# Kernel optimization log

Hardware: AMD Instinct MI355X
Metric: run time of the kernel (lower is better)

The kernel has to match this reference:

```python
import jax, jax.numpy as jnp
import numpy as np

C_DIM = 128
HIDDEN = 128
RESO = 128
PADDING = 0.1


def _resnet_block(x, w0, b0, w1, b1, ws):
    # ResnetBlockFC: net = fc_0(relu(x)); dx = fc_1(relu(net)); out = shortcut(x) + dx
    net = jnp.maximum(x, 0.0) @ w0 + b0
    dx = jnp.maximum(net, 0.0) @ w1 + b1
    return x @ ws + dx


def _scatter_mean(c, index, num_seg):
    # c: (B, T, C) float, index: (B, T) int -> (B, num_seg, C), empty bins stay 0
    def one(cb, ib):
        s = jax.ops.segment_sum(cb, ib, num_segments=num_seg)
        cnt = jax.ops.segment_sum(jnp.ones((cb.shape[0],), cb.dtype), ib, num_segments=num_seg)
        return s / jnp.maximum(cnt, 1.0)[:, None]
    return jax.vmap(one)(c, index)


def setup_inputs() -> dict:
    key = jax.random.key(0)
    ks = jax.random.split(key, 12)
    B, T, D = 2, 65536, 3
    h = HIDDEN
    p = jax.random.uniform(ks[0], (B, T, D), jnp.float32, minval=-0.5, maxval=0.5)
    s = 0.02
    fc_pos_w = jax.random.normal(ks[1], (D, 2 * h), jnp.float32) * s
    fc_pos_b = jax.random.normal(ks[2], (2 * h,), jnp.float32) * s
    # 5 ResnetBlockFC blocks, all (2h -> h) since c_dim == hidden_dim
    w0 = jax.random.normal(ks[3], (5, 2 * h, h), jnp.float32) * s
    b0 = jax.random.normal(ks[4], (5, h), jnp.float32) * s
    w1 = jax.random.normal(ks[5], (5, h, h), jnp.float32) * s
    b1 = jax.random.normal(ks[6], (5, h), jnp.float32) * s
    ws = jax.random.normal(ks[7], (5, 2 * h, h), jnp.float32) * s  # shortcut, no bias
    return {"p": p, "fc_pos_w": fc_pos_w, "fc_pos_b": fc_pos_b,
            "w0": w0, "b0": b0, "w1": w1, "b1": b1, "ws": ws}


def reference(p, fc_pos_w, fc_pos_b, w0, b0, w1, b1, ws):
    # PointNet ResNet encoder
    net = p @ fc_pos_w + fc_pos_b  # (B, T, 2h)
    for i in range(5):
        hfeat = _resnet_block(net, w0[i], b0[i], w1[i], b1[i], ws[i])  # (B, T, h)
        if i < 4:
            pooled = jnp.max(hfeat, axis=1, keepdims=True)
            net = jnp.concatenate([hfeat, jnp.broadcast_to(pooled, hfeat.shape)], axis=-1)
    c = hfeat  # (B, T, c_dim)

    # normalize_coordinate(plane='xz'): take dims (0, 2), map to [0, 1)
    xy = p[..., jnp.array([0, 2])]
    xy = xy / (1.0 + PADDING + 1e-3) + 0.5
    xy = jnp.clip(xy, 0.0, 1.0 - 1e-6)
    # coordinate2index
    xi = (xy * RESO).astype(jnp.int32)
    index = xi[..., 0] + RESO * xi[..., 1]  # (B, T)

    fea = _scatter_mean(c, index, RESO * RESO)  # (B, R*R, c_dim)
    fea_plane = jnp.transpose(fea, (0, 2, 1)).reshape(p.shape[0], C_DIM, RESO, RESO)
    return fea_plane
```

## Files before the change

kernel.cpp:

```cpp
#include <hip/hip_runtime.h>
#include <hip/hip_bf16.h>


#define G_ALL 131072
#define HD    128
#define NBINS 16384

typedef __attribute__((ext_vector_type(8))) short short8;
typedef __attribute__((ext_vector_type(4))) float f32x4;

#define MFMA16(a, b, c) __builtin_amdgcn_mfma_f32_16x16x32_bf16(a, b, c, 0, 0, 0)

__device__ __forceinline__ float bf16_to_f32(unsigned short u) {
  union { unsigned int u; float f; } v; v.u = ((unsigned int)u) << 16; return v.f;
}
__device__ __forceinline__ unsigned short f32_to_bf16(float f) {
  union { float f; unsigned int u; } v; v.f = f;
  unsigned int u = v.u;
  u += 0x7fffu + ((u >> 16) & 1u);
  return (unsigned short)(u >> 16);
}
__device__ __forceinline__ unsigned int f32_key(float f) {
  union { float f; unsigned int u; } v; v.f = f;
  return (v.u & 0x80000000u) ? ~v.u : (v.u | 0x80000000u);
}
__device__ __forceinline__ float key_f32(unsigned int k) {
  union { unsigned int u; float f; } v;
  v.u = (k & 0x80000000u) ? (k & 0x7fffffffu) : ~k;
  return v.f;
}
__device__ __forceinline__ int bin_of(float p0, float p2) {
  float x = p0 / 1.101f + 0.5f;
  x = fminf(fmaxf(x, 0.0f), 1.0f - 1e-6f);
  int xi = (int)(x * 128.0f);
  float z = p2 / 1.101f + 0.5f;
  z = fminf(fmaxf(z, 0.0f), 1.0f - 1e-6f);
  int zi = (int)(z * 128.0f);
  return xi + 128 * zi;
}
__device__ __forceinline__ short8 relu8(short8 a) {
  short8 r;
#pragma unroll
  for (int e = 0; e < 8; e++) r[e] = a[e] < 0 ? (short)0 : a[e];
  return r;
}

__global__ void prep_kernel(const float* __restrict__ fcw,
                            const float* __restrict__ fcb,
                            const float* __restrict__ ws0,
                            float* __restrict__ Sp, float* __restrict__ bsp,
                            unsigned int* __restrict__ pool,
                            int* __restrict__ hist) {
  int j = threadIdx.x;
  for (int d = 0; d < 3; d++) {
    float s = 0.f;
    for (int ch = 0; ch < 256; ch++)
      s = fmaf(fcw[d * 256 + ch], ws0[ch * HD + j], s);
    Sp[d * HD + j] = s;
  }
  float s = 0.f;
  for (int ch = 0; ch < 256; ch++)
    s = fmaf(fcb[ch], ws0[ch * HD + j], s);
  bsp[j] = s;
  for (int k = j; k < 4 * 2 * 128; k += 128) pool[k] = 0u;
  for (int k = j; k < 2 * NBINS; k += 128) hist[k] = 0;
}

__global__ void wprep_kernel(const float* __restrict__ w0,
                             const float* __restrict__ w1,
                             const float* __restrict__ ws,
                             unsigned short* __restrict__ B0t,
                             unsigned short* __restrict__ W0t,
                             unsigned short* __restrict__ W1t,
                             unsigned short* __restrict__ WSt) {
  int gid = blockIdx.x * 256 + threadIdx.x;
  float v;
  unsigned short* dstp;
  int dst;
  if (gid < 32768) {
    int n = gid >> 8, k = gid & 255;
    v = w0[k * 128 + n];
    dstp = B0t; dst = gid;
  } else if (gid < 98304) {
    int i = gid - 32768; int s = i >> 14; int n = (i >> 7) & 127; int k = i & 127;
    v = w0[(size_t)((s + 1) * 256 + k) * 128 + n];
    dstp = W0t; dst = i;
  } else if (gid < 180224) {
    int i = gid - 98304; int s = i >> 14; int n = (i >> 7) & 127; int k = i & 127;
    v = w1[(size_t)(s * 128 + k) * 128 + n];
    dstp = W1t; dst = i;
  } else if (gid < 245760) {
    int i = gid - 180224; int s = i >> 14; int n = (i >> 7) & 127; int k = i & 127;
    v = ws[(size_t)((s + 1) * 256 + k) * 128 + n];
    dstp = WSt; dst = i;
  } else return;
  dstp[dst] = f32_to_bf16(v);
}

__global__ __launch_bounds__(256) void index_kernel(const float* __restrict__ p,
                                                    int* __restrict__ hist) {
  int g = blockIdx.x * 256 + threadIdx.x;
  int b = g >> 16;
  int idx = bin_of(p[3 * (size_t)g], p[3 * (size_t)g + 2]);
  atomicAdd(&hist[b * NBINS + idx], 1);
}

__global__ __launch_bounds__(1024) void scan_kernel(int* __restrict__ hist,
                                                    int* __restrict__ offsets) {
  __shared__ int sd[1024];
  int t = threadIdx.x;
  int vals[32];
  int s = 0;
#pragma unroll
  for (int i = 0; i < 32; i++) { vals[i] = hist[t * 32 + i]; s += vals[i]; }
  sd[t] = s;
  __syncthreads();
  for (int d = 1; d < 1024; d <<= 1) {
    int v = (t >= d) ? sd[t - d] : 0;
    __syncthreads();
    sd[t] += v;
    __syncthreads();
  }
  int run = sd[t] - s;
#pragma unroll
  for (int i = 0; i < 32; i++) {
    offsets[t * 32 + i] = run;
    hist[t * 32 + i] = run;
    run += vals[i];
  }
  if (t == 1023) offsets[32768] = run;
}

__global__ __launch_bounds__(256) void fill_kernel(const float* __restrict__ p,
                                                   int* __restrict__ cursor,
                                                   int* __restrict__ order) {
  int g = blockIdx.x * 256 + threadIdx.x;
  int b = g >> 16;
  int idx = bin_of(p[3 * (size_t)g], p[3 * (size_t)g + 2]);
  int pos = atomicAdd(&cursor[b * NBINS + idx], 1);
  order[pos] = g;
}

__global__ __launch_bounds__(256) void gather_kernel(
    const unsigned short* __restrict__ c, const int* __restrict__ offsets,
    const int* __restrict__ order, float* __restrict__ out) {
  __shared__ float acc[129 * 65];
  const int tid = threadIdx.x;
  const int wave = tid >> 6, lane = tid & 63;
  const int B0 = blockIdx.x * 64;
  const int b = B0 >> 14;

  for (int bi = 0; bi < 16; bi++) {
    const int binL = wave * 16 + bi;
    const int B = B0 + binL;
    const int st = offsets[B], en = offsets[B + 1];
    float a0 = 0.f, a1 = 0.f;
    for (int k = st; k < en; k++) {
      int g = order[k];
      unsigned int u = *(const unsigned int*)(c + (size_t)g * HD + lane * 2);
      a0 += bf16_to_f32((unsigned short)(u & 0xffffu));
      a1 += bf16_to_f32((unsigned short)(u >> 16));
    }
    acc[(2 * lane) * 65 + binL] = a0;
    acc[(2 * lane + 1) * 65 + binL] = a1;
    if (lane == 0) acc[128 * 65 + binL] = (float)(en - st);
  }
  __syncthreads();

  const size_t outBase = (size_t)b * HD * NBINS + (size_t)(B0 & (NBINS - 1));
  const float cnt = fmaxf(acc[128 * 65 + lane], 1.0f);
#pragma unroll
  for (int c2 = 0; c2 < 32; c2++) {
    int ch = wave * 32 + c2;
    out[outBase + (size_t)ch * NBINS + lane] = acc[ch * 65 + lane] / cnt;
  }
}

__global__ __launch_bounds__(512, 4) void stage0_kernel(
    const float* __restrict__ p, const float* __restrict__ fcw,
    const float* __restrict__ fcb,
    const unsigned short* __restrict__ B0t,
    const unsigned short* __restrict__ W1t,
    const float* __restrict__ b0, const float* __restrict__ b1,
    const float* __restrict__ Sp, const float* __restrict__ bsp,
    unsigned short* __restrict__ hout, unsigned int* __restrict__ pool) {
  __shared__ float fcL[1024];
  __shared__ float ptL[64 * 5];
  __shared__ unsigned short x0t[64 * 264];
  __shared__ unsigned short m2[64 * 136];
  const int tid = threadIdx.x;
  const int lane = tid & 63;
  const int q = lane >> 4, l15 = lane & 15;
  const int nt = tid >> 6;
  const int b = blockIdx.x >> 8;
  const int wrow = nt * 16 + l15;

  short8 b0w[8], w1w[4];
#pragma unroll
  for (int kc = 0; kc < 8; kc++)
    b0w[kc] = *(const short8*)(B0t + (size_t)wrow * 256 + kc * 32 + q * 8);
#pragma unroll
  for (int kc = 0; kc < 4; kc++)
    w1w[kc] = *(const short8*)(W1t + (size_t)wrow * 128 + kc * 32 + q * 8);
  const float bias1 = b0[wrow];
  const float bias2 = bsp[wrow] + b1[wrow];
  const float sp0 = Sp[wrow], sp1 = Sp[128 + wrow], sp2 = Sp[256 + wrow];

  for (int k = tid; k < 1024; k += 512)
    fcL[k] = (k < 768) ? fcw[k] : fcb[k - 768];

  for (int it = 0; it < 4; it++) {
    const int rowBase = (blockIdx.x * 4 + it) * 64;
    __syncthreads();
    if (tid < 192) ptL[(tid / 3) * 5 + (tid % 3)] = p[(size_t)rowBase * 3 + tid];
    {
      int row = tid >> 3, c8 = tid & 7;
      const float* pr = p + (size_t)(rowBase + row) * 3;
      float p0 = pr[0], p1 = pr[1], p2 = pr[2];
#pragma unroll
      for (int cc = 0; cc < 32; cc++) {
        int ch = c8 + cc * 8;
        float x = fcL[768 + ch] + p0 * fcL[ch] + p1 * fcL[256 + ch] + p2 * fcL[512 + ch];
        x0t[row * 264 + ch] = f32_to_bf16(fmaxf(x, 0.f));
      }
    }
    __syncthreads();
    f32x4 C1[4];
#pragma unroll
    for (int s = 0; s < 4; s++) C1[s] = (f32x4){bias1, bias1, bias1, bias1};
#pragma unroll
    for (int kc = 0; kc < 8; kc++) {
#pragma unroll
      for (int s = 0; s < 4; s++) {
        short8 Ar = *(const short8*)(&x0t[(s * 16 + l15) * 264 + kc * 32 + q * 8]);
        C1[s] = MFMA16(Ar, b0w[kc], C1[s]);
      }
    }
#pragma unroll
    for (int s = 0; s < 4; s++)
#pragma unroll
      for (int r = 0; r < 4; r++)
        m2[(s * 16 + q * 4 + r) * 136 + nt * 16 + l15] =
            f32_to_bf16(fmaxf(C1[s][r], 0.f));
    __syncthreads();
    f32x4 C2[4];
#pragma unroll
    for (int s = 0; s < 4; s++)
#pragma unroll
      for (int r = 0; r < 4; r++) {
        int row = s * 16 + q * 4 + r;
        C2[s][r] = bias2 + ptL[row * 5] * sp0 + ptL[row * 5 + 1] * sp1 +
                   ptL[row * 5 + 2] * sp2;
      }
#pragma unroll
    for (int kc = 0; kc < 4; kc++) {
#pragma unroll
      for (int s = 0; s < 4; s++) {
        short8 Am = *(const short8*)(&m2[(s * 16 + l15) * 136 + kc * 32 + q * 8]);
        C2[s] = MFMA16(Am, w1w[kc], C2[s]);
      }
    }
#pragma unroll
    for (int s = 0; s < 4; s++)
#pragma unroll
      for (int r = 0; r < 4; r++)
        x0t[(s * 16 + q * 4 + r) * 136 + nt * 16 + l15] = f32_to_bf16(C2[s][r]);
    {
      float m = -1e30f;
#pragma unroll
      for (int s = 0; s < 4; s++)
#pragma unroll
        for (int r = 0; r < 4; r++) m = fmaxf(m, C2[s][r]);
      m = fmaxf(m, __shfl_xor(m, 16, 64));
      m = fmaxf(m, __shfl_xor(m, 32, 64));
      if (lane < 16) atomicMax(&pool[b * 128 + nt * 16 + lane], f32_key(m));
    }
    __syncthreads();
    {
      int r = tid >> 3, cs = (tid & 7) * 16;
      short8 v0 = *(const short8*)(&x0t[r * 136 + cs]);
      short8 v1 = *(const short8*)(&x0t[r * 136 + cs + 8]);
      *(short8*)(hout + (size_t)(rowBase + r) * 128 + cs) = v0;
      *(short8*)(hout + (size_t)(rowBase + r) * 128 + cs + 8) = v1;
    }
  }
}

__global__ __launch_bounds__(512, 4) void stageN_kernel(
    const unsigned short* __restrict__ hin, unsigned short* __restrict__ hout,
    const unsigned short* __restrict__ W0t,
    const unsigned short* __restrict__ W1t,
    const unsigned short* __restrict__ WSt,
    const float* __restrict__ b0e, const float* __restrict__ bse,
    unsigned int* __restrict__ pool, int doPool) {
  __shared__ unsigned short At[64 * 136];
  __shared__ unsigned short m2[64 * 136];
  const int tid = threadIdx.x;
  const int lane = tid & 63;
  const int q = lane >> 4, l15 = lane & 15;
  const int nt = tid >> 6;
  const int b = blockIdx.x >> 8;
  const int wrow = nt * 16 + l15;

  short8 w0w[4], w1w[4], wsw[4];
#pragma unroll
  for (int kc = 0; kc < 4; kc++) {
    w0w[kc] = *(const short8*)(W0t + (size_t)wrow * 128 + kc * 32 + q * 8);
    w1w[kc] = *(const short8*)(W1t + (size_t)wrow * 128 + kc * 32 + q * 8);
    wsw[kc] = *(const short8*)(WSt + (size_t)wrow * 128 + kc * 32 + q * 8);
  }
  const float bias1 = b0e[b * 128 + wrow];
  const float bias2 = bse[b * 128 + wrow];
  const int r8 = tid >> 3, cs8 = (tid & 7) * 16;

  for (int it = 0; it < 4; it++) {
    const int rowBase = (blockIdx.x * 4 + it) * 64;
    __syncthreads();
    {
      const size_t gb = ((size_t)rowBase + r8) * 128 + cs8;
      short8 v0 = *(const short8*)(hin + gb);
      short8 v1 = *(const short8*)(hin + gb + 8);
      *(short8*)(&At[r8 * 136 + cs8]) = v0;
      *(short8*)(&At[r8 * 136 + cs8 + 8]) = v1;
    }
    __syncthreads();
    f32x4 C1[4], C2[4];
#pragma unroll
    for (int s = 0; s < 4; s++) {
      C1[s] = (f32x4){bias1, bias1, bias1, bias1};
      C2[s] = (f32x4){bias2, bias2, bias2, bias2};
    }
#pragma unroll
    for (int kc = 0; kc < 4; kc++) {
#pragma unroll
      for (int s = 0; s < 4; s++) {
        short8 Ah = *(const short8*)(&At[(s * 16 + l15) * 136 + kc * 32 + q * 8]);
        short8 Ar = relu8(Ah);
        C1[s] = MFMA16(Ar, w0w[kc], C1[s]);
        C2[s] = MFMA16(Ah, wsw[kc], C2[s]);
      }
    }
#pragma unroll
    for (int s = 0; s < 4; s++)
#pragma unroll
      for (int r = 0; r < 4; r++)
        m2[(s * 16 + q * 4 + r) * 136 + nt * 16 + l15] =
            f32_to_bf16(fmaxf(C1[s][r], 0.f));
    __syncthreads();
#pragma unroll
    for (int kc = 0; kc < 4; kc++) {
#pragma unroll
      for (int s = 0; s < 4; s++) {
        short8 Am = *(const short8*)(&m2[(s * 16 + l15) * 136 + kc * 32 + q * 8]);
        C2[s] = MFMA16(Am, w1w[kc], C2[s]);
      }
    }
    if (doPool) {
      float m = -1e30f;
#pragma unroll
      for (int s = 0; s < 4; s++)
#pragma unroll
        for (int r = 0; r < 4; r++) m = fmaxf(m, C2[s][r]);
      m = fmaxf(m, __shfl_xor(m, 16, 64));
      m = fmaxf(m, __shfl_xor(m, 32, 64));
      if (lane < 16) atomicMax(&pool[b * 128 + nt * 16 + lane], f32_key(m));
    }
#pragma unroll
    for (int s = 0; s < 4; s++)
#pragma unroll
      for (int r = 0; r < 4; r++)
        At[(s * 16 + q * 4 + r) * 136 + nt * 16 + l15] = f32_to_bf16(C2[s][r]);
    __syncthreads();
    {
      short8 v0 = *(const short8*)(&At[r8 * 136 + cs8]);
      short8 v1 = *(const short8*)(&At[r8 * 136 + cs8 + 8]);
      *(short8*)(hout + (size_t)(rowBase + r8) * 128 + cs8) = v0;
      *(short8*)(hout + (size_t)(rowBase + r8) * 128 + cs8 + 8) = v1;
    }
  }
}

__global__ void fold_kernel(const unsigned int* __restrict__ pool,
                            const float* __restrict__ b0s,
                            const float* __restrict__ b1s,
                            const float* __restrict__ w0hi,
                            const float* __restrict__ wshi,
                            float* __restrict__ b0e, float* __restrict__ bse) {
  __shared__ float ps[256];
  int tid = threadIdx.x;
  int b = tid >> 7, j = tid & 127;
  ps[tid] = key_f32(pool[tid]);
  __syncthreads();
  float a0 = b0s[j], a1 = b1s[j];
  for (int ch = 0; ch < 128; ch++) {
    float pv = ps[b * 128 + ch];
    a0 = fmaf(fmaxf(pv, 0.f), w0hi[ch * HD + j], a0);
    a1 = fmaf(pv, wshi[ch * HD + j], a1);
  }
  b0e[b * 128 + j] = a0;
  bse[b * 128 + j] = a1;
}

extern "C" void kernel_launch(void* const* d_in, const int* in_sizes, int n_in,
                              void* d_out, int out_size, void* d_ws,
                              size_t ws_size, hipStream_t stream) {
  const float* p   = (const float*)d_in[0];
  const float* fcw = (const float*)d_in[1];
  const float* fcb = (const float*)d_in[2];
  const float* w0  = (const float*)d_in[3];
  const float* b0  = (const float*)d_in[4];
  const float* w1  = (const float*)d_in[5];
  const float* b1  = (const float*)d_in[6];
  const float* wsc = (const float*)d_in[7];
  float* out = (float*)d_out;

  char* wsp = (char*)d_ws;
  unsigned short* hA = (unsigned short*)wsp;
  unsigned short* hB = hA + (size_t)G_ALL * HD;
  unsigned short* B0t = hB + (size_t)G_ALL * HD;
  unsigned short* W0t = B0t + 32768;
  unsigned short* W1t = W0t + 65536;
  unsigned short* WSt = W1t + 81920;
  unsigned int* pool = (unsigned int*)(WSt + 65536);
  float* b0e = (float*)(pool + 1024);
  float* bse = b0e + 1024;
  float* Sp  = bse + 1024;
  float* bsp = Sp + 384;
  int* hist    = (int*)(bsp + 128);
  int* offsets = hist + 2 * NBINS;
  int* order   = offsets + 2 * NBINS + 4;

  prep_kernel<<<1, 128, 0, stream>>>(fcw, fcb, wsc, Sp, bsp, pool, hist);
  wprep_kernel<<<960, 256, 0, stream>>>(w0, w1, wsc, B0t, W0t, W1t, WSt);
  index_kernel<<<512, 256, 0, stream>>>(p, hist);
  scan_kernel<<<1, 1024, 0, stream>>>(hist, offsets);
  fill_kernel<<<512, 256, 0, stream>>>(p, hist, order);

  stage0_kernel<<<512, 512, 0, stream>>>(p, fcw, fcb, B0t, W1t,
                                         b0, b1, Sp, bsp, hA, pool);
  unsigned short* hin = hA;
  unsigned short* hout = hB;
  for (int s = 1; s < 5; s++) {
    fold_kernel<<<1, 256, 0, stream>>>(
        pool + (s - 1) * 256, b0 + s * HD, b1 + s * HD,
        w0 + (size_t)(s * 256 + 128) * HD, wsc + (size_t)(s * 256 + 128) * HD,
        b0e + (s - 1) * 256, bse + (s - 1) * 256);
    stageN_kernel<<<512, 512, 0, stream>>>(
        hin, hout, W0t + (s - 1) * 16384, W1t + s * 16384,
        WSt + (s - 1) * 16384, b0e + (s - 1) * 256, bse + (s - 1) * 256,
        pool + s * 256, (s < 4) ? 1 : 0);
    unsigned short* t = hin; hin = hout; hout = t;
  }
  gather_kernel<<<512, 256, 0, stream>>>(hin, offsets, order, out);
}
```

Baseline: 401.5 us.

## Scatter final stage rows into bin-sorted order and fuse prep kernels

```diff
diff --git a/kernel.cpp b/kernel.cpp
--- a/kernel.cpp
+++ b/kernel.cpp
@@ -45,35 +45,44 @@
   return r;
 }
 
-__global__ void prep_kernel(const float* __restrict__ fcw,
-                            const float* __restrict__ fcb,
-                            const float* __restrict__ ws0,
-                            float* __restrict__ Sp, float* __restrict__ bsp,
-                            unsigned int* __restrict__ pool,
-                            int* __restrict__ hist) {
-  int j = threadIdx.x;
-  for (int d = 0; d < 3; d++) {
+__global__ __launch_bounds__(128) void prep_kernel(
+    const float* __restrict__ fcw, const float* __restrict__ fcb,
+    const float* __restrict__ ws0, float* __restrict__ Sp,
+    float* __restrict__ bsp, unsigned int* __restrict__ pool,
+    int* __restrict__ hist) {
+  int t = blockIdx.x * 128 + threadIdx.x;
+  hist[t * 2] = 0;
+  hist[t * 2 + 1] = 0;
+  if (t < 1024) pool[t] = 0u;
+  if (blockIdx.x == 0) {
+    int j = threadIdx.x;
+    for (int d = 0; d < 3; d++) {
+      float s = 0.f;
+      for (int ch = 0; ch < 256; ch++)
+        s = fmaf(fcw[d * 256 + ch], ws0[ch * HD + j], s);
+      Sp[d * HD + j] = s;
+    }
     float s = 0.f;
     for (int ch = 0; ch < 256; ch++)
-      s = fmaf(fcw[d * 256 + ch], ws0[ch * HD + j], s);
-    Sp[d * HD + j] = s;
-  }
-  float s = 0.f;
-  for (int ch = 0; ch < 256; ch++)
-    s = fmaf(fcb[ch], ws0[ch * HD + j], s);
-  bsp[j] = s;
-  for (int k = j; k < 4 * 2 * 128; k += 128) pool[k] = 0u;
-  for (int k = j; k < 2 * NBINS; k += 128) hist[k] = 0;
-}
-
-__global__ void wprep_kernel(const float* __restrict__ w0,
-                             const float* __restrict__ w1,
-                             const float* __restrict__ ws,
-                             unsigned short* __restrict__ B0t,
-                             unsigned short* __restrict__ W0t,
-                             unsigned short* __restrict__ W1t,
-                             unsigned short* __restrict__ WSt) {
+      s = fmaf(fcb[ch], ws0[ch * HD + j], s);
+    bsp[j] = s;
+  }
+}
+
+__global__ __launch_bounds__(256) void wi_kernel(
+    const float* __restrict__ w0, const float* __restrict__ w1,
+    const float* __restrict__ ws, const float* __restrict__ p,
+    unsigned short* __restrict__ B0t, unsigned short* __restrict__ W0t,
+    unsigned short* __restrict__ W1t, unsigned short* __restrict__ WSt,
+    int* __restrict__ hist) {
   int gid = blockIdx.x * 256 + threadIdx.x;
+  if (gid >= 245760) {
+    int g = gid - 245760;
+    int b = g >> 16;
+    int idx = bin_of(p[3 * (size_t)g], p[3 * (size_t)g + 2]);
+    atomicAdd(&hist[b * NBINS + idx], 1);
+    return;
+  }
   float v;
   unsigned short* dstp;
   int dst;
@@ -89,20 +98,12 @@
     int i = gid - 98304; int s = i >> 14; int n = (i >> 7) & 127; int k = i & 127;
     v = w1[(size_t)(s * 128 + k) * 128 + n];
     dstp = W1t; dst = i;
-  } else if (gid < 245760) {
+  } else {
     int i = gid - 180224; int s = i >> 14; int n = (i >> 7) & 127; int k = i & 127;
     v = ws[(size_t)((s + 1) * 256 + k) * 128 + n];
     dstp = WSt; dst = i;
-  } else return;
+  }
   dstp[dst] = f32_to_bf16(v);
-}
-
-__global__ __launch_bounds__(256) void index_kernel(const float* __restrict__ p,
-                                                    int* __restrict__ hist) {
-  int g = blockIdx.x * 256 + threadIdx.x;
-  int b = g >> 16;
-  int idx = bin_of(p[3 * (size_t)g], p[3 * (size_t)g + 2]);
-  atomicAdd(&hist[b * NBINS + idx], 1);
 }
 
 __global__ __launch_bounds__(1024) void scan_kernel(int* __restrict__ hist,
@@ -133,17 +134,17 @@
 
 __global__ __launch_bounds__(256) void fill_kernel(const float* __restrict__ p,
                                                    int* __restrict__ cursor,
-                                                   int* __restrict__ order) {
+                                                   int* __restrict__ rank) {
   int g = blockIdx.x * 256 + threadIdx.x;
   int b = g >> 16;
   int idx = bin_of(p[3 * (size_t)g], p[3 * (size_t)g + 2]);
   int pos = atomicAdd(&cursor[b * NBINS + idx], 1);
-  order[pos] = g;
+  rank[g] = pos;
 }
 
 __global__ __launch_bounds__(256) void gather_kernel(
-    const unsigned short* __restrict__ c, const int* __restrict__ offsets,
-    const int* __restrict__ order, float* __restrict__ out) {
+    const unsigned short* __restrict__ cS, const int* __restrict__ offsets,
+    float* __restrict__ out) {
   __shared__ float acc[129 * 65];
   const int tid = threadIdx.x;
   const int wave = tid >> 6, lane = tid & 63;
@@ -155,9 +156,17 @@
     const int B = B0 + binL;
     const int st = offsets[B], en = offsets[B + 1];
     float a0 = 0.f, a1 = 0.f;
-    for (int k = st; k < en; k++) {
-      int g = order[k];
-      unsigned int u = *(const unsigned int*)(c + (size_t)g * HD + lane * 2);
+    int k = st;
+    for (; k + 2 <= en; k += 2) {
+      unsigned int u0 = *(const unsigned int*)(cS + (size_t)k * HD + lane * 2);
+      unsigned int u1 = *(const unsigned int*)(cS + (size_t)(k + 1) * HD + lane * 2);
+      a0 += bf16_to_f32((unsigned short)(u0 & 0xffffu));
+      a1 += bf16_to_f32((unsigned short)(u0 >> 16));
+      a0 += bf16_to_f32((unsigned short)(u1 & 0xffffu));
+      a1 += bf16_to_f32((unsigned short)(u1 >> 16));
+    }
+    if (k < en) {
+      unsigned int u = *(const unsigned int*)(cS + (size_t)k * HD + lane * 2);
       a0 += bf16_to_f32((unsigned short)(u & 0xffffu));
       a1 += bf16_to_f32((unsigned short)(u >> 16));
     }
@@ -292,7 +301,8 @@
     const unsigned short* __restrict__ W1t,
     const unsigned short* __restrict__ WSt,
     const float* __restrict__ b0e, const float* __restrict__ bse,
-    unsigned int* __restrict__ pool, int doPool) {
+    unsigned int* __restrict__ pool, int doPool,
+    const int* __restrict__ rank, int useRank) {
   __shared__ unsigned short At[64 * 136];
   __shared__ unsigned short m2[64 * 136];
   const int tid = threadIdx.x;
@@ -372,10 +382,12 @@
         At[(s * 16 + q * 4 + r) * 136 + nt * 16 + l15] = f32_to_bf16(C2[s][r]);
     __syncthreads();
     {
+      int destRow = rowBase + r8;
+      if (useRank) destRow = rank[destRow];
       short8 v0 = *(const short8*)(&At[r8 * 136 + cs8]);
       short8 v1 = *(const short8*)(&At[r8 * 136 + cs8 + 8]);
-      *(short8*)(hout + (size_t)(rowBase + r8) * 128 + cs8) = v0;
-      *(short8*)(hout + (size_t)(rowBase + r8) * 128 + cs8 + 8) = v1;
+      *(short8*)(hout + (size_t)destRow * 128 + cs8) = v0;
+      *(short8*)(hout + (size_t)destRow * 128 + cs8 + 8) = v1;
     }
   }
 }
@@ -428,13 +440,12 @@
   float* bsp = Sp + 384;
   int* hist    = (int*)(bsp + 128);
   int* offsets = hist + 2 * NBINS;
-  int* order   = offsets + 2 * NBINS + 4;
-
-  prep_kernel<<<1, 128, 0, stream>>>(fcw, fcb, wsc, Sp, bsp, pool, hist);
-  wprep_kernel<<<960, 256, 0, stream>>>(w0, w1, wsc, B0t, W0t, W1t, WSt);
-  index_kernel<<<512, 256, 0, stream>>>(p, hist);
+  int* rank    = offsets + 2 * NBINS + 4;
+
+  prep_kernel<<<128, 128, 0, stream>>>(fcw, fcb, wsc, Sp, bsp, pool, hist);
+  wi_kernel<<<1472, 256, 0, stream>>>(w0, w1, wsc, p, B0t, W0t, W1t, WSt, hist);
   scan_kernel<<<1, 1024, 0, stream>>>(hist, offsets);
-  fill_kernel<<<512, 256, 0, stream>>>(p, hist, order);
+  fill_kernel<<<512, 256, 0, stream>>>(p, hist, rank);
 
   stage0_kernel<<<512, 512, 0, stream>>>(p, fcw, fcb, B0t, W1t,
                                          b0, b1, Sp, bsp, hA, pool);
@@ -448,8 +459,8 @@
     stageN_kernel<<<512, 512, 0, stream>>>(
         hin, hout, W0t + (s - 1) * 16384, W1t + s * 16384,
         WSt + (s - 1) * 16384, b0e + (s - 1) * 256, bse + (s - 1) * 256,
-        pool + s * 256, (s < 4) ? 1 : 0);
+        pool + s * 256, (s < 4) ? 1 : 0, rank, (s == 4) ? 1 : 0);
     unsigned short* t = hin; hin = hout; hout = t;
   }
-  gather_kernel<<<512, 256, 0, stream>>>(hin, offsets, order, out);
-}
+  gather_kernel<<<512, 256, 0, stream>>>(hin, offsets, out);
+}
```

Result: faster. 357.6 us (-10.9%).
